# Kernel tuning notes

Measured on AMD Instinct MI355X. Metric: run time of the kernel, lower is better.

Reference implementation:

```python
import jax, jax.numpy as jnp
import numpy as np
import math

NUM_HEADS = 3
WINDOW = 7


def _shift_masks(ws):
    # row_mask: block mask for windows wrapping across the bottom edge
    half = ws * (ws // 2)  # 21 for ws=7
    row = np.zeros((ws * ws, ws * ws), np.float32)
    row[-half:, :-half] = -np.inf
    row[:-half, -half:] = -np.inf
    # column_mask = rearrange(row, '(r w1) (c w2) -> (w1 r) (w2 c)')
    col = row.reshape(ws, ws, ws, ws).transpose(1, 0, 3, 2).reshape(ws * ws, ws * ws)
    return jnp.asarray(row), jnp.asarray(col)


def setup_inputs() -> dict:
    key = jax.random.key(0)
    ks = jax.random.split(key, 5)
    B, S, E = 64, 3136, 96
    return {
        'x': jax.random.normal(ks[0], (B, S, E), jnp.float32),
        'w1': jax.random.normal(ks[1], (3 * E, E), jnp.float32) * 0.05,
        'b1': jax.random.normal(ks[2], (3 * E,), jnp.float32) * 0.05,
        'w2': jax.random.normal(ks[3], (E, E), jnp.float32) * 0.05,
        'b2': jax.random.normal(ks[4], (E,), jnp.float32) * 0.05,
    }


def reference(x, w1, b1, w2, b2):
    b, S, E = x.shape
    h = w = int(math.sqrt(S))          # 56
    ws = WINDOW
    H = NUM_HEADS
    Eh = E // H                        # head dim = 32
    nh, nw = h // ws, w // ws          # windows per axis = 8
    scale = 1.0 / math.sqrt(E / H)
    # faithful to original: forward shift = -ws//2 = -4, inverse shift = ws//2 = 3
    shift_fwd = -ws // 2
    shift_bwd = ws // 2

    qkv = x @ w1.T + b1                              # [b, S, 3E]
    qkv = qkv.reshape(b, h, w, E, 3)                 # (c K) split, K fastest
    qkv = jnp.roll(qkv, (shift_fwd, shift_fwd), axis=(1, 2))
    # b (nh m1) (nw m2) (H Eh) K -> b H nh nw (m1 m2) Eh K
    qkv = qkv.reshape(b, nh, ws, nw, ws, H, Eh, 3)
    qkv = qkv.transpose(0, 5, 1, 3, 2, 4, 6, 7).reshape(b, H, nh, nw, ws * ws, Eh, 3)
    Q, K, V = qkv[..., 0], qkv[..., 1], qkv[..., 2]

    s = jnp.einsum('bHhwme,bHhwne->bHhwmn', Q, K) * scale  # [b,H,nh,nw,49,49]
    row_mask, col_mask = _shift_masks(ws)
    s = s.at[:, :, -1, :].add(row_mask)   # last row of windows
    s = s.at[:, :, :, -1].add(col_mask)   # last column of windows

    att = jax.nn.softmax(s, axis=-1)
    o = jnp.einsum('bHhwmn,bHhwne->bHhwme', att, V)        # [b,H,nh,nw,49,Eh]
    # b H nh nw (m1 m2) Eh -> b (nh m1) (nw m2) (H Eh)
    o = o.reshape(b, H, nh, nw, ws, ws, Eh)
    o = o.transpose(0, 2, 4, 3, 5, 1, 6).reshape(b, h, w, E)
    o = jnp.roll(o, (shift_bwd, shift_bwd), axis=(1, 2))
    o = o.reshape(b, S, E)
    return o @ w2.T + b2
```

## Files before the change

### kernel.cpp

```cpp
#include <hip/hip_runtime.h>


typedef _Float16 f16;
typedef _Float16 f16x2 __attribute__((ext_vector_type(2)));
typedef _Float16 f16x4 __attribute__((ext_vector_type(4)));
typedef _Float16 f16x8 __attribute__((ext_vector_type(8)));
typedef float f32x4 __attribute__((ext_vector_type(4)));

static __device__ __forceinline__ f32x4 mfma16(f16x8 a, f16x8 b, f32x4 c) {
    return __builtin_amdgcn_mfma_f32_16x16x32_f16(a, b, c, 0, 0, 0);
}
static __device__ __forceinline__ f16x8 cvt8(const float* __restrict__ p) {
    float4 f0 = *(const float4*)(p);
    float4 f1 = *(const float4*)(p + 4);
    f16x8 h;
    h[0]=(f16)f0.x; h[1]=(f16)f0.y; h[2]=(f16)f0.z; h[3]=(f16)f0.w;
    h[4]=(f16)f1.x; h[5]=(f16)f1.y; h[6]=(f16)f1.z; h[7]=(f16)f1.w;
    return h;
}
static __device__ __forceinline__ f16x8 cvt8p(const float4& f0, const float4& f1) {
    f16x8 h;
    h[0]=(f16)f0.x; h[1]=(f16)f0.y; h[2]=(f16)f0.z; h[3]=(f16)f0.w;
    h[4]=(f16)f1.x; h[5]=(f16)f1.y; h[6]=(f16)f1.z; h[7]=(f16)f1.w;
    return h;
}

#define QK_STR 100
#define VT_STR 60
#define SMEM_BYTES 31136
#define OFF_K  9800
#define OFF_VT 19600

union U2 { int i; f16x2 h; };
union U8 { int i[4]; f16x8 h; };

template<bool WS>
__global__ __launch_bounds__(256, 4) void swin_fused(
    const float* __restrict__ x, const float* __restrict__ w1,
    const float* __restrict__ b1, const float* __restrict__ w2,
    const float* __restrict__ b2, float* __restrict__ out,
    const f16* __restrict__ w1p, const f16* __restrict__ w2p,
    const float* __restrict__ b1p)
{
    __shared__ __align__(16) char smem[SMEM_BYTES];
    f16* q_s  = (f16*)(smem);
    f16* k_s  = (f16*)(smem + OFF_K);
    f16* vt_s = (f16*)(smem + OFF_VT);
    f16* o_s  = q_s;

    const int tid  = threadIdx.x;
    const int wv   = tid >> 6;
    const int lane = tid & 63;
    const int lrow = lane & 15;
    const int lq   = lane >> 4;

    const int bx = blockIdx.x;
    const int b  = bx >> 6;
    const int wz = bx & 63;
    const int wh = wz >> 3;
    const int ww = wz & 7;

    const float* xb = x + b * (3136 * 96);

    if (tid < 96) {
        #pragma unroll
        for (int p7 = 49; p7 < 60; ++p7) vt_s[tid * VT_STR + p7] = (f16)0.f;
    }
    if (tid < 8) vt_s[96 * VT_STR + tid] = (f16)0.f;

    {
        f16x8 bf[5][3];
        int   kq[5], cb[5];
        #pragma unroll
        for (int t = 0; t < 5; ++t) {
            int ot = wv + 4 * t;
            if (ot < 18) {
                int kqv = ot / 6;
                kq[t] = kqv;
                cb[t] = (ot - kqv * 6) * 16;
                if constexpr (WS) {
                    #pragma unroll
                    for (int ks = 0; ks < 3; ++ks)
                        bf[t][ks] = *(const f16x8*)(w1p + (ot*16 + lrow)*96 + ks*32 + lq*8);
                } else {
                    int srowA = (ot*16 + lrow - kqv*96) * 3 + kqv;
                    #pragma unroll
                    for (int ks = 0; ks < 3; ++ks)
                        bf[t][ks] = cvt8(w1 + srowA*96 + ks*32 + lq*8);
                }
            } else kq[t] = -1;
        }
        const float* xrow[4];
        #pragma unroll
        for (int pt = 0; pt < 4; ++pt) {
            int p  = pt * 16 + lrow;
            int pc = (p < 49) ? p : 48;
            int i  = pc / 7, j = pc - i * 7;
            int r  = wh * 7 + i + 4; if (r >= 56) r -= 56;
            int c  = ww * 7 + j + 4; if (c >= 56) c -= 56;
            xrow[pt] = xb + (r * 56 + c) * 96;
        }
        float4 xbuf0[3][2], xbuf1[3][2];
        #pragma unroll
        for (int ks = 0; ks < 3; ++ks) {
            xbuf0[ks][0] = *(const float4*)(xrow[0] + ks * 32 + lq * 8);
            xbuf0[ks][1] = *(const float4*)(xrow[0] + ks * 32 + lq * 8 + 4);
        }
        #pragma unroll
        for (int pt = 0; pt < 4; ++pt) {
            float4 (*cur)[2] = (pt & 1) ? xbuf1 : xbuf0;
            float4 (*nxt)[2] = (pt & 1) ? xbuf0 : xbuf1;
            if (pt < 3) {
                #pragma unroll
                for (int ks = 0; ks < 3; ++ks) {
                    nxt[ks][0] = *(const float4*)(xrow[pt+1] + ks * 32 + lq * 8);
                    nxt[ks][1] = *(const float4*)(xrow[pt+1] + ks * 32 + lq * 8 + 4);
                }
            }
            f16x8 xf[3];
            #pragma unroll
            for (int ks = 0; ks < 3; ++ks) xf[ks] = cvt8p(cur[ks][0], cur[ks][1]);
            const int  p   = pt * 16 + lrow;
            const bool pok = (p < 49);
            #pragma unroll
            for (int t = 0; t < 5; ++t) {
                if (kq[t] < 0) continue;
                int ot = wv + 4 * t;
                f32x4 acc = {0.f, 0.f, 0.f, 0.f};
                if (kq[t] == 2) {
                    #pragma unroll
                    for (int ks = 0; ks < 3; ++ks) acc = mfma16(xf[ks], bf[t][ks], acc);
                    float bc;
                    if constexpr (WS) bc = b1p[ot*16 + lrow];
                    else              bc = b1[(ot*16 + lrow - 192)*3 + 2];
                    int cc = cb[t] + lrow;
                    f16x4 pk;
                    #pragma unroll
                    for (int i2 = 0; i2 < 4; ++i2) pk[i2] = (f16)(acc[i2] + bc);
                    int p4 = pt * 16 + lq * 4;
                    if (p4 < 45)       *(f16x4*)(vt_s + cc * VT_STR + p4) = pk;
                    else if (p4 == 48) vt_s[cc * VT_STR + 48] = pk[0];
                } else {
                    #pragma unroll
                    for (int ks = 0; ks < 3; ++ks) acc = mfma16(bf[t][ks], xf[ks], acc);
                    if (pok) {
                        f32x4 br;
                        if constexpr (WS) {
                            br = *(const f32x4*)(b1p + ot*16 + lq*4);
                        } else {
                            #pragma unroll
                            for (int i2 = 0; i2 < 4; ++i2)
                                br[i2] = b1[(ot*16 + lq*4 + i2 - kq[t]*96)*3 + kq[t]];
                        }
                        f16x4 pk;
                        #pragma unroll
                        for (int i2 = 0; i2 < 4; ++i2) pk[i2] = (f16)(acc[i2] + br[i2]);
                        f16* dst = (kq[t] == 0 ? q_s : k_s) + p * QK_STR + cb[t] + lq * 4;
                        *(f16x4*)dst = pk;
                    }
                }
            }
        }
    }
    __syncthreads();

    const bool mrow = (wh == 7), mcol = (ww == 7);
    const float scale = 0.17677669529663687f;
    const int m = wv * 16 + lrow;

    float mv[16];
    {
        const bool am = (m >= 28);
        const bool a4 = (m % 7) >= 4;
        #pragma unroll
        for (int nt = 0; nt < 4; ++nt)
            #pragma unroll
            for (int i2 = 0; i2 < 4; ++i2) {
                int nn = nt * 16 + lq * 4 + i2;
                bool ok = (nn < 49)
                       && (!mrow || (am == (nn >= 28)))
                       && (!mcol || (a4 == ((nn % 7) >= 4)));
                mv[nt*4 + i2] = ok ? 0.f : -3e38f;
            }
    }
    const int idxA = lrow + 32 * (lq & 1);
    const int idxB = idxA + 16;

    f16x8 bq[3];
    #pragma unroll
    for (int hh = 0; hh < 3; ++hh)
        bq[hh] = *(const f16x8*)(q_s + m * QK_STR + hh * 32 + lq * 8);

    f32x4 acc2[6];
    #pragma unroll
    for (int ot2 = 0; ot2 < 6; ++ot2) acc2[ot2] = f32x4{0.f, 0.f, 0.f, 0.f};

    f32x4 sc[4];
    #pragma unroll
    for (int nt = 0; nt < 4; ++nt) {
        f16x8 ak = *(const f16x8*)(k_s + (nt*16 + lrow)*QK_STR + lq*8);
        f32x4 z = {0.f, 0.f, 0.f, 0.f};
        sc[nt] = mfma16(ak, bq[0], z);
    }

    #pragma unroll
    for (int hh = 0; hh < 3; ++hh) {
        f16x8 akn[4];
        if (hh < 2) {
            #pragma unroll
            for (int nt = 0; nt < 4; ++nt)
                akn[nt] = *(const f16x8*)(k_s + (nt*16 + lrow)*QK_STR + (hh+1)*32 + lq*8);
        }
        f16x8 va[2][2];
        #pragma unroll
        for (int et = 0; et < 2; ++et) {
            int vrow = hh * 32 + et * 16 + lrow;
            va[et][0] = *(const f16x8*)(vt_s + vrow * VT_STR + lq * 8);
            va[et][1] = *(const f16x8*)(vt_s + vrow * VT_STR + 32 + lq * 8);
        }
        float ev[16];
        #pragma unroll
        for (int nt = 0; nt < 4; ++nt)
            #pragma unroll
            for (int i2 = 0; i2 < 4; ++i2)
                ev[nt*4 + i2] = fmaf(sc[nt][i2], scale, mv[nt*4 + i2]);
        float tm[8];
        #pragma unroll
        for (int k2 = 0; k2 < 8; ++k2) tm[k2] = fmaxf(ev[2*k2], ev[2*k2+1]);
        #pragma unroll
        for (int k2 = 0; k2 < 4; ++k2) tm[k2] = fmaxf(tm[k2], tm[k2+4]);
        float vm = fmaxf(fmaxf(tm[0], tm[1]), fmaxf(tm[2], tm[3]));
        vm = fmaxf(vm, __shfl_xor(vm, 16));
        vm = fmaxf(vm, __shfl_xor(vm, 32));
        #pragma unroll
        for (int k2 = 0; k2 < 16; ++k2) ev[k2] = __expf(ev[k2] - vm);
        float ts[8];
        #pragma unroll
        for (int k2 = 0; k2 < 8; ++k2) ts[k2] = ev[2*k2] + ev[2*k2+1];
        #pragma unroll
        for (int k2 = 0; k2 < 4; ++k2) ts[k2] += ts[k2+4];
        float s = (ts[0] + ts[1]) + (ts[2] + ts[3]);
        s += __shfl_xor(s, 16);
        s += __shfl_xor(s, 32);
        float inv = 1.0f / s;

        int pd[4][2];
        #pragma unroll
        for (int nt = 0; nt < 4; ++nt) {
            U2 u0, u1;
            u0.h[0] = (f16)ev[nt*4+0]; u0.h[1] = (f16)ev[nt*4+1];
            u1.h[0] = (f16)ev[nt*4+2]; u1.h[1] = (f16)ev[nt*4+3];
            pd[nt][0] = u0.i; pd[nt][1] = u1.i;
        }
        U8 ub0, ub1;
        #pragma unroll
        for (int w = 0; w < 4; ++w) {
            int idx = (w < 2) ? idxA : idxB;
            int rr  = w & 1;
            int a0v = __shfl(pd[0][rr], idx);
            int a1v = __shfl(pd[1][rr], idx);
            ub0.i[w] = (lq & 2) ? a1v : a0v;
            int c0v = __shfl(pd[2][rr], idx);
            int c1v = __shfl(pd[3][rr], idx);
            ub1.i[w] = (lq & 2) ? c1v : c0v;
        }
        #pragma unroll
        for (int et = 0; et < 2; ++et) {
            f32x4 z = {0.f, 0.f, 0.f, 0.f};
            f32x4 oc = mfma16(va[et][0], ub0.h, z);
            oc = mfma16(va[et][1], ub1.h, oc);
            if (m < 49) {
                f16x4 pk;
                #pragma unroll
                for (int i2 = 0; i2 < 4; ++i2) pk[i2] = (f16)(oc[i2] * inv);
                *(f16x4*)(o_s + m * QK_STR + hh * 32 + et * 16 + lq * 4) = pk;
            }
        }
        {
            f16x8 aw_h[6];
            #pragma unroll
            for (int ot2 = 0; ot2 < 6; ++ot2) {
                if constexpr (WS)
                    aw_h[ot2] = *(const f16x8*)(w2p + (ot2*16 + lrow)*96 + hh*32 + lq*8);
                else
                    aw_h[ot2] = cvt8(w2 + (ot2*16 + lrow)*96 + hh*32 + lq*8);
            }
            f16x8 bo_h = *(const f16x8*)(o_s + m * QK_STR + hh * 32 + lq * 8);
            #pragma unroll
            for (int ot2 = 0; ot2 < 6; ++ot2)
                acc2[ot2] = mfma16(aw_h[ot2], bo_h, acc2[ot2]);
        }
        if (hh < 2) {
            #pragma unroll
            for (int nt = 0; nt < 4; ++nt) {
                f32x4 z = {0.f, 0.f, 0.f, 0.f};
                sc[nt] = mfma16(akn[nt], bq[hh+1], z);
            }
        }
    }

    {
        int mm2 = (m < 49) ? m : 48;
        int i = mm2 / 7, j = mm2 - i * 7;
        int orow = wh * 7 + i + 3; if (orow >= 56) orow -= 56;
        int ocol = ww * 7 + j + 3; if (ocol >= 56) ocol -= 56;
        float* op = out + (size_t)(b * 3136 + orow * 56 + ocol) * 96;
        #pragma unroll
        for (int ot2 = 0; ot2 < 6; ++ot2) {
            f32x4 bias = *(const f32x4*)(b2 + ot2 * 16 + lq * 4);
            if (m < 49) {
                f32x4 o4 = acc2[ot2] + bias;
                *(f32x4*)(op + ot2 * 16 + lq * 4) = o4;
            }
        }
    }
}

__global__ void prep_weights(const float* __restrict__ w1, const float* __restrict__ b1,
                             const float* __restrict__ w2,
                             f16* __restrict__ w1p, f16* __restrict__ w2p,
                             float* __restrict__ b1p)
{
    int idx = blockIdx.x * 256 + threadIdx.x;
    if (idx < 27648) {
        int np = idx / 96, k = idx - np * 96;
        int kq = np / 96, c96 = np - kq * 96;
        w1p[idx] = (f16)w1[(c96 * 3 + kq) * 96 + k];
    } else if (idx < 36864) {
        int i2 = idx - 27648;
        w2p[i2] = (f16)w2[i2];
    } else if (idx < 37152) {
        int np = idx - 36864;
        int kq = np / 96, c96 = np - kq * 96;
        b1p[np] = b1[c96 * 3 + kq];
    }
}

extern "C" void kernel_launch(void* const* d_in, const int* in_sizes, int n_in,
                              void* d_out, int out_size, void* d_ws, size_t ws_size,
                              hipStream_t stream) {
    const float* x  = (const float*)d_in[0];
    const float* w1 = (const float*)d_in[1];
    const float* b1 = (const float*)d_in[2];
    const float* w2 = (const float*)d_in[3];
    const float* b2 = (const float*)d_in[4];
    float* out = (float*)d_out;

    const size_t need = 27648u * 2 + 9216u * 2 + 288u * 4;
    if (ws_size >= need) {
        f16*   w1p = (f16*)d_ws;
        f16*   w2p = w1p + 27648;
        float* b1p = (float*)(w2p + 9216);
        prep_weights<<<dim3(146), dim3(256), 0, stream>>>(w1, b1, w2, w1p, w2p, b1p);
        swin_fused<true><<<dim3(4096), dim3(256), 0, stream>>>(
            x, w1, b1, w2, b2, out, w1p, w2p, b1p);
    } else {
        swin_fused<false><<<dim3(4096), dim3(256), 0, stream>>>(
            x, w1, b1, w2, b2, out, nullptr, nullptr, nullptr);
    }
}
```

Before: 254.9 us.

## Defer output projection to epilogue with double-buffered W2 loads and MFMA priority

Moves the per-head output-projection MFMAs out of the head loop into a final epilogue. The epilogue reads the full attention output row from LDS and loops over output tiles, double-buffering W2 fragment loads from global memory. This frees the six live f32x4 accumulators during the head loop, lowering register pressure. It also raises wave priority around MFMA bursts with s_setprio. The trade-off is an extra serial epilogue phase with global loads that may not be fully hidden.

New measurement: 251.2 us. No clear change (-1.5%).

```diff
diff --git a/kernel.cpp b/kernel.cpp
--- a/kernel.cpp
+++ b/kernel.cpp
@@ -191,17 +191,24 @@
     for (int hh = 0; hh < 3; ++hh)
         bq[hh] = *(const f16x8*)(q_s + m * QK_STR + hh * 32 + lq * 8);
 
-    f32x4 acc2[6];
+    f16x8 aw0[3], aw1[3];
     #pragma unroll
-    for (int ot2 = 0; ot2 < 6; ++ot2) acc2[ot2] = f32x4{0.f, 0.f, 0.f, 0.f};
+    for (int ks = 0; ks < 3; ++ks) {
+        if constexpr (WS)
+            aw0[ks] = *(const f16x8*)(w2p + lrow*96 + ks*32 + lq*8);
+        else
+            aw0[ks] = cvt8(w2 + lrow*96 + ks*32 + lq*8);
+    }
 
     f32x4 sc[4];
+    __builtin_amdgcn_s_setprio(1);
     #pragma unroll
     for (int nt = 0; nt < 4; ++nt) {
         f16x8 ak = *(const f16x8*)(k_s + (nt*16 + lrow)*QK_STR + lq*8);
         f32x4 z = {0.f, 0.f, 0.f, 0.f};
         sc[nt] = mfma16(ak, bq[0], z);
     }
+    __builtin_amdgcn_s_setprio(0);
 
     #pragma unroll
     for (int hh = 0; hh < 3; ++hh) {
@@ -264,6 +271,7 @@
             int c1v = __shfl(pd[3][rr], idx);
             ub1.i[w] = (lq & 2) ? c1v : c0v;
         }
+        __builtin_amdgcn_s_setprio(1);
         #pragma unroll
         for (int et = 0; et < 2; ++et) {
             f32x4 z = {0.f, 0.f, 0.f, 0.f};
@@ -276,20 +284,6 @@
                 *(f16x4*)(o_s + m * QK_STR + hh * 32 + et * 16 + lq * 4) = pk;
             }
         }
-        {
-            f16x8 aw_h[6];
-            #pragma unroll
-            for (int ot2 = 0; ot2 < 6; ++ot2) {
-                if constexpr (WS)
-                    aw_h[ot2] = *(const f16x8*)(w2p + (ot2*16 + lrow)*96 + hh*32 + lq*8);
-                else
-                    aw_h[ot2] = cvt8(w2 + (ot2*16 + lrow)*96 + hh*32 + lq*8);
-            }
-            f16x8 bo_h = *(const f16x8*)(o_s + m * QK_STR + hh * 32 + lq * 8);
-            #pragma unroll
-            for (int ot2 = 0; ot2 < 6; ++ot2)
-                acc2[ot2] = mfma16(aw_h[ot2], bo_h, acc2[ot2]);
-        }
         if (hh < 2) {
             #pragma unroll
             for (int nt = 0; nt < 4; ++nt) {
@@ -297,19 +291,41 @@
                 sc[nt] = mfma16(akn[nt], bq[hh+1], z);
             }
         }
+        __builtin_amdgcn_s_setprio(0);
     }
 
     {
+        f16x8 bo[3];
+        #pragma unroll
+        for (int ks = 0; ks < 3; ++ks)
+            bo[ks] = *(const f16x8*)(o_s + m * QK_STR + ks * 32 + lq * 8);
         int mm2 = (m < 49) ? m : 48;
         int i = mm2 / 7, j = mm2 - i * 7;
         int orow = wh * 7 + i + 3; if (orow >= 56) orow -= 56;
         int ocol = ww * 7 + j + 3; if (ocol >= 56) ocol -= 56;
         float* op = out + (size_t)(b * 3136 + orow * 56 + ocol) * 96;
+
         #pragma unroll
         for (int ot2 = 0; ot2 < 6; ++ot2) {
+            f16x8* cw = (ot2 & 1) ? aw1 : aw0;
+            f16x8* nw = (ot2 & 1) ? aw0 : aw1;
+            if (ot2 < 5) {
+                #pragma unroll
+                for (int ks = 0; ks < 3; ++ks) {
+                    if constexpr (WS)
+                        nw[ks] = *(const f16x8*)(w2p + ((ot2+1)*16 + lrow)*96 + ks*32 + lq*8);
+                    else
+                        nw[ks] = cvt8(w2 + ((ot2+1)*16 + lrow)*96 + ks*32 + lq*8);
+                }
+            }
+            f32x4 acc = {0.f, 0.f, 0.f, 0.f};
+            __builtin_amdgcn_s_setprio(1);
+            #pragma unroll
+            for (int ks = 0; ks < 3; ++ks) acc = mfma16(cw[ks], bo[ks], acc);
+            __builtin_amdgcn_s_setprio(0);
             f32x4 bias = *(const f32x4*)(b2 + ot2 * 16 + lq * 4);
             if (m < 49) {
-                f32x4 o4 = acc2[ot2] + bias;
+                f32x4 o4 = acc + bias;
                 *(f32x4*)(op + ot2 * 16 + lq * 4) = o4;
             }
         }
```
